# Performance work log

Hardware: AMD Instinct MI355X
Metric: run time of the kernel (lower is better)

Reference implementation:

```python
import jax, jax.numpy as jnp
import numpy as np

B, L, H, N = 16, 4096, 256, 64
N2 = N // 2


def setup_inputs() -> dict:
    key = jax.random.key(0)
    ks = jax.random.split(key, 12)
    x = jax.random.normal(ks[0], (B, L, H), dtype=jnp.float32)
    # S4D kernel params (S4D-Lin init)
    log_dt = jax.random.uniform(ks[1], (H,), dtype=jnp.float32) * (
        np.log(0.1) - np.log(0.001)) + np.log(0.001)
    log_A_real = jnp.full((H, N2), jnp.log(0.5), dtype=jnp.float32)
    A_imag = jnp.broadcast_to(np.pi * jnp.arange(N2, dtype=jnp.float32), (H, N2)).copy()
    C_re = jax.random.normal(ks[2], (H, N2), dtype=jnp.float32) * (0.5 ** 0.5)
    C_im = jax.random.normal(ks[3], (H, N2), dtype=jnp.float32) * (0.5 ** 0.5)
    D = jax.random.normal(ks[4], (H,), dtype=jnp.float32)
    # LayerNorm + 2-layer MLP params
    ln_g = jnp.ones((H,), dtype=jnp.float32)
    ln_b = jnp.zeros((H,), dtype=jnp.float32)
    s = 1.0 / np.sqrt(H)
    W1 = jax.random.uniform(ks[5], (H, H), dtype=jnp.float32, minval=-s, maxval=s)
    b1 = jax.random.uniform(ks[6], (H,), dtype=jnp.float32, minval=-s, maxval=s)
    W2 = jax.random.uniform(ks[7], (H, H), dtype=jnp.float32, minval=-s, maxval=s)
    b2 = jax.random.uniform(ks[8], (H,), dtype=jnp.float32, minval=-s, maxval=s)
    return dict(x=x, log_dt=log_dt, log_A_real=log_A_real, A_imag=A_imag,
                C_re=C_re, C_im=C_im, D=D, ln_g=ln_g, ln_b=ln_b,
                W1=W1, b1=b1, W2=W2, b2=b2)


def _s4d_kernel(log_dt, log_A_real, A_imag, C_re, C_im, length):
    # Returns real convolution kernel of shape (H, length)
    dt = jnp.exp(log_dt)                                  # (H,)
    A = -jnp.exp(log_A_real) + 1j * A_imag                # (H, N2) complex
    C = (C_re + 1j * C_im).astype(jnp.complex64)
    dtA = A * dt[:, None]                                 # (H, N2)
    # Discretization (ZOH-like): C * (exp(dtA) - 1) / A
    Cd = C * (jnp.exp(dtA) - 1.0) / A                     # (H, N2)
    t = jnp.arange(length, dtype=jnp.float32)
    vand = jnp.exp(dtA[:, :, None] * t)                   # (H, N2, L) complex Vandermonde
    K = 2.0 * jnp.einsum('hn,hnl->hl', Cd, vand).real     # (H, L)
    return K


def _forward(x, log_dt, log_A_real, A_imag, C_re, C_im, D,
             ln_g, ln_b, W1, b1, W2, b2):
    Bsz, Lseq, Hdim = x.shape
    K = _s4d_kernel(log_dt, log_A_real, A_imag, C_re, C_im, Lseq)  # (H, L)
    u = jnp.transpose(x, (0, 2, 1))                       # (B, H, L)
    n_fft = 2 * Lseq
    k_f = jnp.fft.rfft(K, n=n_fft)                        # (H, n_fft//2+1)
    u_f = jnp.fft.rfft(u, n=n_fft)                        # (B, H, n_fft//2+1)
    y = jnp.fft.irfft(u_f * k_f, n=n_fft)[..., :Lseq]     # causal conv (B, H, L)
    y = y + u * D[None, :, None]                          # skip connection
    y = jnp.transpose(y, (0, 2, 1))                       # (B, L, H)
    # LayerNorm over H
    mu = jnp.mean(y, axis=-1, keepdims=True)
    var = jnp.mean(jnp.square(y - mu), axis=-1, keepdims=True)
    y = (y - mu) * jax.lax.rsqrt(var + 1e-5) * ln_g + ln_b
    # Linear -> ReLU -> Linear -> ReLU (dropout is identity in eval)
    y = jax.nn.relu(jnp.einsum('blh,oh->blo', y, W1) + b1)
    y = jax.nn.relu(jnp.einsum('blh,oh->blo', y, W2) + b2)
    return x + y


def reference(x, log_dt, log_A_real, A_imag, C_re, C_im, D,
              ln_g, ln_b, W1, b1, W2, b2):
    return _forward(x, log_dt, log_A_real, A_imag, C_re, C_im, D,
                    ln_g, ln_b, W1, b1, W2, b2)
```

## Files before the change

kernel.cpp:

```cpp
#include <hip/hip_runtime.h>

#define H_DIM 256
#define N2D   32
#define L_SEQ 4096
#define B_SZ  16
#define L_C   128
#define N_C   32
#define KPAD  136

typedef short short8 __attribute__((ext_vector_type(8)));
typedef short short4v __attribute__((ext_vector_type(4)));
typedef float f32x4  __attribute__((ext_vector_type(4)));
typedef unsigned short ushort;

__device__ __forceinline__ ushort f2bf(float f) {
  unsigned int u = __float_as_uint(f);
  u = (u + 0x7fffu + ((u >> 16) & 1u)) >> 16;
  return (ushort)u;
}
__device__ __forceinline__ float bf2f(ushort s) {
  return __uint_as_float(((unsigned int)s) << 16);
}

__global__ __launch_bounds__(256) void k_front(
    const float* __restrict__ x, const float* __restrict__ log_dt,
    const float* __restrict__ log_A_real, const float* __restrict__ A_imag,
    const float* __restrict__ C_re, const float* __restrict__ C_im,
    const float* __restrict__ W1, const float* __restrict__ W2,
    const float* __restrict__ gam, const float* __restrict__ bet,
    const float* __restrict__ b1, float* __restrict__ parK,
    ushort* __restrict__ Mb, ushort* __restrict__ Lb,
    ushort* __restrict__ w1f, ushort* __restrict__ w2f,
    float* __restrict__ cs1, float* __restrict__ b1p,
    ushort* __restrict__ U) {
  int bid = blockIdx.x;
  int t = threadIdx.x;
  if (bid < 256) {
    int h = bid;
    __shared__ float sdre[32], sdim[32], scdr[32], scdi[32], slr[32], sli[32];
    if (t < 32) {
      int i = h * 32 + t;
      float dt = expf(log_dt[h]);
      float ar = -expf(log_A_real[i]);
      float ai = A_imag[i];
      float dre = ar * dt, dim = ai * dt;
      float er = expf(dre), sn, cs;
      sincosf(dim, &sn, &cs);
      float lr = er * cs, li = er * sn;
      float nr = lr - 1.f, ni = li;
      float inv = 1.f / (ar * ar + ai * ai);
      float tr = (nr * ar + ni * ai) * inv, ti = (ni * ar - nr * ai) * inv;
      float cdr = C_re[i] * tr - C_im[i] * ti;
      float cdi = C_re[i] * ti + C_im[i] * tr;
      sdre[t] = dre; sdim[t] = dim; scdr[t] = cdr; scdi[t] = cdi;
      slr[t] = lr; sli[t] = li;
      float e1 = expf(128.f * dre), ph = 128.f * dim;
      sincosf(ph, &sn, &cs);
      parK[i] = e1 * cs;
      parK[8192 + i] = e1 * sn;
    }
    __syncthreads();
    if (t < 128) {
      float ksum = 0.f;
      float tf = (float)t;
      for (int n = 0; n < 32; ++n) {
        float e = expf(tf * sdre[n]);
        float sn, cs;
        sincosf(tf * sdim[n], &sn, &cs);
        float pr = e * cs, pi = e * sn;
        ksum = fmaf(scdr[n], pr, fmaf(-scdi[n], pi, ksum));
        Lb[((size_t)h * 64 + 2 * n) * 128 + (127 - t)] = f2bf(pr);
        Lb[((size_t)h * 64 + 2 * n + 1) * 128 + (127 - t)] = f2bf(pi);
        float plr = pr * slr[n] - pi * sli[n];
        float pli = pr * sli[n] + pi * slr[n];
        Mb[((size_t)h * 128 + t) * 64 + 2 * n] =
            f2bf(2.f * (scdr[n] * plr - scdi[n] * pli));
        Mb[((size_t)h * 128 + t) * 64 + 2 * n + 1] =
            f2bf(-2.f * (scdr[n] * pli + scdi[n] * plr));
      }
      parK[16384 + h * 128 + t] = 2.f * ksum;
    }
  } else if (bid < 576) {
    int wb = bid - 256;
    if (wb < 64) {
      int i = wb * 256 + t;
      int mat = i >> 13;
      int fi = i & 8191;
      int l = fi & 63;
      int gk = fi >> 6;
      int g = gk & 15, kk = gk >> 4;
      int srow = mat ? ((g >> 2) * 64 + (l & 15) * 4 + (g & 3))
                     : (g * 16 + (l & 15));
      int scol = kk * 32 + ((l >> 4) << 3);
      const float* W = mat ? W2 : W1;
      ushort* out = mat ? w2f : w1f;
      short8 v;
#pragma unroll
      for (int e = 0; e < 8; ++e) {
        float w = W[(size_t)srow * 256 + scol + e];
        if (!mat) w *= gam[scol + e];
        v[e] = (short)f2bf(w);
      }
      *(short8*)&out[(size_t)fi * 8] = v;
    } else {
      int o = wb - 64;
      __shared__ float ra[256], rb[256];
      float w = W1[(size_t)o * 256 + t];
      ra[t] = bf2f(f2bf(w * gam[t]));
      rb[t] = w * bet[t];
      __syncthreads();
      for (int s = 128; s > 0; s >>= 1) {
        if (t < s) { ra[t] += ra[t + s]; rb[t] += rb[t + s]; }
        __syncthreads();
      }
      if (t == 0) { cs1[o] = ra[0]; b1p[o] = b1[o] + rb[0]; }
    }
  } else {
    int blk = bid - 576;
    int b = blk >> 7;
    int l0 = (blk & 127) << 5;
    __shared__ float tile[32][257];
#pragma unroll 8
    for (int r = 0; r < 32; ++r)
      tile[r][t] = x[((size_t)b * L_SEQ + l0 + r) * H_DIM + t];
    __syncthreads();
    int hq = t >> 2, ls = (t & 3) * 8;
#pragma unroll
    for (int pass = 0; pass < 4; ++pass) {
      int h = pass * 64 + hq;
      short8 v;
#pragma unroll
      for (int j = 0; j < 8; ++j) v[j] = (short)f2bf(tile[ls + j][h]);
      *(short8*)&U[(size_t)h * 65536 + (size_t)b * L_SEQ + l0 + ls] = v;
    }
  }
}

__global__ __launch_bounds__(256, 2) void k_sy(
    const ushort* __restrict__ U, const ushort* __restrict__ Lb,
    const float* __restrict__ parK, const ushort* __restrict__ Mb,
    const float* __restrict__ Dp, ushort* __restrict__ Uo) {
  int wgid = (blockIdx.x & 7) * 128 + (blockIdx.x >> 3);
  int h = wgid >> 2, ct = wgid & 3;
  int t = threadIdx.x;
  int lane = t & 63, wid = t >> 6;
  int wm = wid & 1, wn = wid >> 1;
  int lr_ = lane & 15, lk = (lane >> 4) << 3;
  __shared__ ushort Bt[128][KPAD];
  __shared__ __attribute__((aligned(16))) ushort ovl[18432];
  __shared__ float Krow[128];
  ushort (*sts)[72] = (ushort(*)[72])ovl;
  ushort (*M_lds)[72] = (ushort(*)[72])(ovl + 128 * 72);
  ushort (*T_lds)[136] = (ushort(*)[136])ovl;
  if (t < 128) {
    float kv = parK[16384 + h * 128 + t];
    if (t == 0) kv += Dp[h];
    Krow[t] = kv;
  }
#pragma unroll
  for (int q = 0; q < 8; ++q) {
    int idx = q * 256 + t;
    int cc = idx >> 4, seg = idx & 15;
    int col = ct * 128 + cc;
    int b = col >> 5, c = col & 31;
    *(short8*)&Bt[cc][seg * 8] = *(const short8*)&U[
        (size_t)h * 65536 + (size_t)b * L_SEQ + c * L_C + seg * 8];
  }
#pragma unroll
  for (int q = 0; q < 4; ++q) {
    int idx = q * 256 + t;
    int r = idx >> 3, seg = idx & 7;
    *(short8*)&M_lds[r][seg * 8] =
        *(const short8*)&Mb[((size_t)h * 128 + r) * 64 + seg * 8];
  }
  __syncthreads();
  {
    f32x4 acc2[4][2];
#pragma unroll
    for (int m = 0; m < 4; ++m)
#pragma unroll
      for (int n = 0; n < 2; ++n) acc2[m][n] = (f32x4){0.f, 0.f, 0.f, 0.f};
#pragma unroll
    for (int ks = 0; ks < 4; ++ks) {
      int k0 = ks * 32;
      short8 a[4], bfr[2];
#pragma unroll
      for (int m = 0; m < 4; ++m)
        a[m] = *(const short8*)&Bt[wm * 64 + m * 16 + lr_][k0 + lk];
#pragma unroll
      for (int n = 0; n < 2; ++n)
        bfr[n] = *(const short8*)&Lb[
            ((size_t)h * 64 + wn * 32 + n * 16 + lr_) * 128 + k0 + lk];
#pragma unroll
      for (int m = 0; m < 4; ++m)
#pragma unroll
        for (int n = 0; n < 2; ++n)
          acc2[m][n] = __builtin_amdgcn_mfma_f32_16x16x32_bf16(
              a[m], bfr[n], acc2[m][n], 0, 0, 0);
    }
#pragma unroll
    for (int m = 0; m < 4; ++m)
#pragma unroll
      for (int n = 0; n < 2; ++n)
#pragma unroll
        for (int jj = 0; jj < 4; ++jj) {
          int rowl = wm * 64 + m * 16 + (lane >> 4) * 4 + jj;
          int col2n = wn * 32 + n * 16 + (lane & 15);
          sts[rowl][col2n] = f2bf(acc2[m][n][jj]);
        }
  }
  __syncthreads();
  if (t < 128) {
    int n = t & 31, bl = t >> 5;
    float Lr = parK[h * 32 + n], Li = parK[8192 + h * 32 + n];
    float cr = 0.f, ci = 0.f;
#pragma unroll
    for (int c = 0; c < N_C; ++c) {
      int rowl = bl * 32 + c;
      uint* p = (uint*)&sts[rowl][2 * n];
      uint v = *p;
      float fr = bf2f((ushort)(v & 0xffff));
      float fi = bf2f((ushort)(v >> 16));
      *p = (uint)f2bf(cr) | ((uint)f2bf(ci) << 16);
      float nr_ = fmaf(Lr, cr, fmaf(-Li, ci, fr));
      float ni_ = fmaf(Lr, ci, fmaf(Li, cr, fi));
      cr = nr_; ci = ni_;
    }
  }
  __syncthreads();
  f32x4 acc[4][4];
#pragma unroll
  for (int m = 0; m < 4; ++m)
#pragma unroll
    for (int n = 0; n < 4; ++n) acc[m][n] = (f32x4){0.f, 0.f, 0.f, 0.f};
#pragma unroll
  for (int ks = 0; ks < 2; ++ks) {
    int k0 = ks * 32;
    short8 a[4], bfr[4];
#pragma unroll
    for (int m = 0; m < 4; ++m)
      a[m] = *(const short8*)&sts[wm * 64 + m * 16 + lr_][k0 + lk];
#pragma unroll
    for (int n = 0; n < 4; ++n)
      bfr[n] = *(const short8*)&M_lds[wn * 64 + n * 16 + lr_][k0 + lk];
#pragma unroll
    for (int m = 0; m < 4; ++m)
#pragma unroll
      for (int n = 0; n < 4; ++n)
        acc[m][n] = __builtin_amdgcn_mfma_f32_16x16x32_bf16(a[m], bfr[n],
                                                            acc[m][n], 0, 0, 0);
  }
  __syncthreads();
#pragma unroll
  for (int q = 0; q < 8; ++q) {
    int idx = q * 256 + t;
    int r = idx >> 4, seg = idx & 15;
    short8 v;
#pragma unroll
    for (int e = 0; e < 8; ++e) {
      int d = r - (seg * 8 + e);
      float f = (d >= 0) ? Krow[d] : 0.f;
      v[e] = (short)f2bf(f);
    }
    *(short8*)&T_lds[r][seg * 8] = v;
  }
  __syncthreads();
#pragma unroll
  for (int ks = 0; ks < 4; ++ks) {
    int k0 = ks * 32;
    short8 a[4], bfr[4];
#pragma unroll
    for (int m = 0; m < 4; ++m)
      a[m] = *(const short8*)&Bt[wm * 64 + m * 16 + lr_][k0 + lk];
#pragma unroll
    for (int n = 0; n < 4; ++n)
      bfr[n] = *(const short8*)&T_lds[wn * 64 + n * 16 + lr_][k0 + lk];
#pragma unroll
    for (int m = 0; m < 4; ++m)
#pragma unroll
      for (int n = 0; n < 4; ++n)
        acc[m][n] = __builtin_amdgcn_mfma_f32_16x16x32_bf16(a[m], bfr[n],
                                                            acc[m][n], 0, 0, 0);
  }
  __syncthreads();
#pragma unroll
  for (int m = 0; m < 4; ++m) {
    int rowl = wm * 64 + m * 16 + (lane >> 4) * 4;
#pragma unroll
    for (int jj = 0; jj < 4; ++jj) {
      int row = rowl + jj;
#pragma unroll
      for (int n = 0; n < 4; ++n) {
        int lp = wn * 64 + n * 16 + (lane & 15);
        Bt[row][lp] = f2bf(acc[m][n][jj]);
      }
    }
  }
  __syncthreads();
#pragma unroll
  for (int q = 0; q < 8; ++q) {
    int idx = q * 256 + t;
    int r = idx >> 4, seg = idx & 15;
    int col = ct * 128 + r;
    int b = col >> 5, c = col & 31;
    *(short8*)&Uo[(size_t)h * 65536 + (size_t)b * L_SEQ + c * L_C + seg * 8] =
        *(const short8*)&Bt[r][seg * 8];
  }
}

__global__ __launch_bounds__(512, 4) void k_mlp(
    const ushort* __restrict__ U, const ushort* __restrict__ w1f,
    const ushort* __restrict__ w2f, const float* __restrict__ cs1,
    const float* __restrict__ b1p, const float* __restrict__ b2,
    const float* __restrict__ xres, float* __restrict__ outp) {
  int m0 = blockIdx.x << 7;
  int t = threadIdx.x;
  int lane = t & 63, wid = t >> 6;
  int wm = wid & 1, wn = wid >> 1;
  int lr_ = lane & 15, lk = (lane >> 4) << 3;
  __shared__ ushort smem[33792];
  __shared__ float redA[128][4], redB[128][4];
  __shared__ float mu_s[128], rs_s[128];
  {
    int hseg = t >> 4, l16 = t & 15;
    int sw = (l16 & 7) << 3;
#pragma unroll
    for (int p = 0; p < 8; ++p) {
      int h = p * 32 + hseg;
      short8 v = *(const short8*)&U[(size_t)h * 65536 + m0 + l16 * 8];
      int hx = h ^ sw;
#pragma unroll
      for (int e = 0; e < 8; ++e)
        smem[(l16 * 8 + e) * 264 + hx] = (ushort)v[e];
    }
  }
  __syncthreads();
  {
    int rl = t >> 2, q = (t & 3) << 6;
    float s = 0.f, s2 = 0.f;
#pragma unroll
    for (int e = 0; e < 64; e += 8) {
      short8 v = *(const short8*)&smem[rl * 264 + q + e];
#pragma unroll
      for (int j = 0; j < 8; ++j) {
        float f = bf2f((ushort)v[j]);
        s += f;
        s2 = fmaf(f, f, s2);
      }
    }
    redA[rl][t & 3] = s;
    redB[rl][t & 3] = s2;
  }
  __syncthreads();
  if (t < 128) {
    float ss = redA[t][0] + redA[t][1] + redA[t][2] + redA[t][3];
    float ss2 = redB[t][0] + redB[t][1] + redB[t][2] + redB[t][3];
    float mu = ss * (1.f / 256.f);
    float var = fmaf(ss2, 1.f / 256.f, -mu * mu);
    mu_s[t] = mu;
    rs_s[t] = rsqrtf(var + 1e-5f);
  }
  __syncthreads();
  f32x4 acc[4][4];
#pragma unroll
  for (int m = 0; m < 4; ++m)
#pragma unroll
    for (int n = 0; n < 4; ++n) acc[m][n] = (f32x4){0.f, 0.f, 0.f, 0.f};
#pragma unroll
  for (int kabs = 0; kabs < 8; ++kabs) {
    short8 af[4], bfr[4];
#pragma unroll
    for (int n = 0; n < 4; ++n)
      bfr[n] = *(const short8*)&w1f[(((size_t)kabs * 16 + wn * 4 + n) * 64 +
                                     lane) * 8];
#pragma unroll
    for (int m = 0; m < 4; ++m) {
      int row = wm * 64 + m * 16 + lr_;
      int sw = ((row >> 3) & 7) << 3;
      af[m] = *(const short8*)&smem[row * 264 + ((kabs * 32 + lk) ^ sw)];
    }
#pragma unroll
    for (int m = 0; m < 4; ++m)
#pragma unroll
      for (int n = 0; n < 4; ++n)
        acc[m][n] = __builtin_amdgcn_mfma_f32_16x16x32_bf16(af[m], bfr[n],
                                                            acc[m][n], 0, 0, 0);
  }
  __syncthreads();
  int prow = (lane >> 4) << 2;
  int pcol = lane & 15;
#pragma unroll
  for (int n = 0; n < 4; ++n) {
    int gcol = wn * 64 + n * 16 + pcol;
    float c1v = cs1[gcol], b1v = b1p[gcol];
#pragma unroll
    for (int m = 0; m < 4; ++m) {
      int rbase = wm * 64 + m * 16 + prow;
#pragma unroll
      for (int j = 0; j < 4; ++j) {
        int row = rbase + j;
        float v = fmaxf(
            fmaf(rs_s[row], acc[m][n][j] - mu_s[row] * c1v, b1v), 0.f);
        int byte = ((row << 9) + (gcol << 1)) ^ ((row & 7) << 4);
        smem[byte >> 1] = f2bf(v);
        acc[m][n][j] = 0.f;
      }
    }
  }
  __syncthreads();
#pragma unroll
  for (int kabs = 0; kabs < 8; ++kabs) {
    short8 af[4], bfr[4];
#pragma unroll
    for (int n = 0; n < 4; ++n)
      bfr[n] = *(const short8*)&w2f[(((size_t)kabs * 16 + wn * 4 + n) * 64 +
                                     lane) * 8];
#pragma unroll
    for (int m = 0; m < 4; ++m) {
      int row = wm * 64 + m * 16 + lr_;
      int byte = ((row << 9) + ((kabs * 32 + lk) << 1)) ^ ((row & 7) << 4);
      af[m] = *(const short8*)&smem[byte >> 1];
    }
#pragma unroll
    for (int m = 0; m < 4; ++m)
#pragma unroll
      for (int n = 0; n < 4; ++n)
        acc[m][n] = __builtin_amdgcn_mfma_f32_16x16x32_bf16(af[m], bfr[n],
                                                            acc[m][n], 0, 0, 0);
  }
  f32x4 bv2q = *(const f32x4*)&b2[wn * 64 + pcol * 4];
#pragma unroll
  for (int m = 0; m < 4; ++m) {
#pragma unroll
    for (int j = 0; j < 4; ++j) {
      int grow = m0 + wm * 64 + m * 16 + prow + j;
      size_t base = (size_t)grow * 256 + wn * 64 + pcol * 4;
      f32x4 xr = *(const f32x4*)&xres[base];
      f32x4 o;
#pragma unroll
      for (int n = 0; n < 4; ++n)
        o[n] = xr[n] + fmaxf(acc[m][n][j] + bv2q[n], 0.f);
      *(f32x4*)&outp[base] = o;
    }
  }
}

extern "C" void kernel_launch(void* const* d_in, const int* in_sizes, int n_in,
                              void* d_out, int out_size, void* d_ws, size_t ws_size,
                              hipStream_t stream) {
  const float* x          = (const float*)d_in[0];
  const float* log_dt     = (const float*)d_in[1];
  const float* log_A_real = (const float*)d_in[2];
  const float* A_imag     = (const float*)d_in[3];
  const float* C_re       = (const float*)d_in[4];
  const float* C_im       = (const float*)d_in[5];
  const float* Dp         = (const float*)d_in[6];
  const float* ln_g       = (const float*)d_in[7];
  const float* ln_b       = (const float*)d_in[8];
  const float* W1         = (const float*)d_in[9];
  const float* b1         = (const float*)d_in[10];
  const float* W2         = (const float*)d_in[11];
  const float* b2         = (const float*)d_in[12];

  char* ws = (char*)d_ws;
  float* parK = (float*)ws;
  float* cs1  = (float*)(ws + 0x30000);
  float* b1p  = (float*)(ws + 0x30400);
  ushort* w1f = (ushort*)(ws + 0x40000);
  ushort* w2f = (ushort*)(ws + 0x60000);
  ushort* Mb  = (ushort*)(ws + 0x80000);
  ushort* Lb  = (ushort*)(ws + 0x480000);
  ushort* U   = (ushort*)(ws + 0x2080000);

  k_front<<<2624, 256, 0, stream>>>(x, log_dt, log_A_real, A_imag, C_re, C_im,
                                    W1, W2, ln_g, ln_b, b1, parK, Mb, Lb,
                                    w1f, w2f, cs1, b1p, U);
  k_sy<<<1024, 256, 0, stream>>>(U, Lb, parK, Mb, Dp, U);
  k_mlp<<<512, 512, 0, stream>>>(U, w1f, w2f, cs1, b1p, b2, x,
                                 (float*)d_out);
}
```

Before: 93.41 us.

## Split MLP block into two 64-row chunks with prefetch and lighter barriers

The k_mlp kernel now handles its 128 rows as two 64-row chunks. The U loads for the second chunk are prefetched into registers while the first chunk is processed, and the residual x loads are issued before the first GEMM. LayerNorm statistics are reduced with wave shuffles instead of shared-memory partial arrays. __syncthreads is replaced by an lgkmcnt wait plus s_barrier, and the LDS layout gets a new XOR swizzle with less padding. The goal is to overlap global loads with compute and cut LDS and register use, at the cost of more barrier phases and smaller per-chunk MFMA tiles.

```diff
diff --git a/kernel.cpp b/kernel.cpp
--- a/kernel.cpp
+++ b/kernel.cpp
@@ -20,6 +20,10 @@
 }
 __device__ __forceinline__ float bf2f(ushort s) {
   return __uint_as_float(((unsigned int)s) << 16);
+}
+__device__ __forceinline__ void barlg() {
+  asm volatile("s_waitcnt lgkmcnt(0)" ::: "memory");
+  __builtin_amdgcn_s_barrier();
 }
 
 __global__ __launch_bounds__(256) void k_front(
@@ -318,129 +322,153 @@
   int lane = t & 63, wid = t >> 6;
   int wm = wid & 1, wn = wid >> 1;
   int lr_ = lane & 15, lk = (lane >> 4) << 3;
-  __shared__ ushort smem[33792];
-  __shared__ float redA[128][4], redB[128][4];
-  __shared__ float mu_s[128], rs_s[128];
-  {
-    int hseg = t >> 4, l16 = t & 15;
-    int sw = (l16 & 7) << 3;
-#pragma unroll
-    for (int p = 0; p < 8; ++p) {
-      int h = p * 32 + hseg;
-      short8 v = *(const short8*)&U[(size_t)h * 65536 + m0 + l16 * 8];
-      int hx = h ^ sw;
-#pragma unroll
-      for (int e = 0; e < 8; ++e)
-        smem[(l16 * 8 + e) * 264 + hx] = (ushort)v[e];
-    }
-  }
-  __syncthreads();
-  {
-    int rl = t >> 2, q = (t & 3) << 6;
-    float s = 0.f, s2 = 0.f;
-#pragma unroll
-    for (int e = 0; e < 64; e += 8) {
-      short8 v = *(const short8*)&smem[rl * 264 + q + e];
-#pragma unroll
-      for (int j = 0; j < 8; ++j) {
-        float f = bf2f((ushort)v[j]);
-        s += f;
-        s2 = fmaf(f, f, s2);
-      }
-    }
-    redA[rl][t & 3] = s;
-    redB[rl][t & 3] = s2;
-  }
-  __syncthreads();
-  if (t < 128) {
-    float ss = redA[t][0] + redA[t][1] + redA[t][2] + redA[t][3];
-    float ss2 = redB[t][0] + redB[t][1] + redB[t][2] + redB[t][3];
-    float mu = ss * (1.f / 256.f);
-    float var = fmaf(ss2, 1.f / 256.f, -mu * mu);
-    mu_s[t] = mu;
-    rs_s[t] = rsqrtf(var + 1e-5f);
-  }
-  __syncthreads();
-  f32x4 acc[4][4];
-#pragma unroll
-  for (int m = 0; m < 4; ++m)
-#pragma unroll
-    for (int n = 0; n < 4; ++n) acc[m][n] = (f32x4){0.f, 0.f, 0.f, 0.f};
-#pragma unroll
-  for (int kabs = 0; kabs < 8; ++kabs) {
-    short8 af[4], bfr[4];
-#pragma unroll
-    for (int n = 0; n < 4; ++n)
-      bfr[n] = *(const short8*)&w1f[(((size_t)kabs * 16 + wn * 4 + n) * 64 +
-                                     lane) * 8];
-#pragma unroll
-    for (int m = 0; m < 4; ++m) {
-      int row = wm * 64 + m * 16 + lr_;
-      int sw = ((row >> 3) & 7) << 3;
-      af[m] = *(const short8*)&smem[row * 264 + ((kabs * 32 + lk) ^ sw)];
-    }
-#pragma unroll
-    for (int m = 0; m < 4; ++m)
-#pragma unroll
-      for (int n = 0; n < 4; ++n)
-        acc[m][n] = __builtin_amdgcn_mfma_f32_16x16x32_bf16(af[m], bfr[n],
-                                                            acc[m][n], 0, 0, 0);
-  }
-  __syncthreads();
-  int prow = (lane >> 4) << 2;
-  int pcol = lane & 15;
+  __shared__ __attribute__((aligned(16))) ushort sm[32768];
+  __shared__ float mu_s[64], rs_s[64];
+  int prow = (lane >> 4) << 2, pcol = lane & 15;
+  float c1v[4], b1v[4];
 #pragma unroll
   for (int n = 0; n < 4; ++n) {
     int gcol = wn * 64 + n * 16 + pcol;
-    float c1v = cs1[gcol], b1v = b1p[gcol];
-#pragma unroll
-    for (int m = 0; m < 4; ++m) {
-      int rbase = wm * 64 + m * 16 + prow;
+    c1v[n] = cs1[gcol];
+    b1v[n] = b1p[gcol];
+  }
+  f32x4 b2q = *(const f32x4*)&b2[wn * 64 + pcol * 4];
+  int hseg = t >> 3, l8 = t & 7;
+  short8 uv[4];
+#pragma unroll
+  for (int p = 0; p < 4; ++p)
+    uv[p] = *(const short8*)&U[(size_t)(p * 64 + hseg) * 65536 + m0 + l8 * 8];
+#pragma unroll
+  for (int c = 0; c < 2; ++c) {
+    int mc = m0 + c * 64;
+#pragma unroll
+    for (int p = 0; p < 4; ++p) {
+      int h = p * 64 + hseg;
+#pragma unroll
+      for (int e = 0; e < 8; ++e) {
+        int m = l8 * 8 + e;
+        int byte = m * 512 + ((h * 2) ^ ((e ^ l8) << 4));
+        sm[byte >> 1] = (ushort)uv[p][e];
+      }
+    }
+    if (c == 0) {
+#pragma unroll
+      for (int p = 0; p < 4; ++p)
+        uv[p] = *(const short8*)&U[(size_t)(p * 64 + hseg) * 65536 + m0 + 64 +
+                                   l8 * 8];
+    }
+    barlg();
+    {
+      int row = t >> 3, c8 = t & 7;
+      int fr = ((row & 7) ^ ((row >> 3) & 7)) << 4;
+      float s = 0.f, s2 = 0.f;
+#pragma unroll
+      for (int e = 0; e < 4; ++e) {
+        int byte = row * 512 + (((c8 + e * 8) * 16) ^ fr);
+        short8 v = *(const short8*)&sm[byte >> 1];
+#pragma unroll
+        for (int j = 0; j < 8; ++j) {
+          float f = bf2f((ushort)v[j]);
+          s += f;
+          s2 = fmaf(f, f, s2);
+        }
+      }
+#pragma unroll
+      for (int d = 1; d < 8; d <<= 1) {
+        s += __shfl_xor(s, d);
+        s2 += __shfl_xor(s2, d);
+      }
+      if (c8 == 0) {
+        float mu = s * (1.f / 256.f);
+        float var = fmaf(s2, 1.f / 256.f, -mu * mu);
+        mu_s[row] = mu;
+        rs_s[row] = rsqrtf(var + 1e-5f);
+      }
+    }
+    barlg();
+    f32x4 xr[2][4];
+#pragma unroll
+    for (int m = 0; m < 2; ++m)
+#pragma unroll
+      for (int j = 0; j < 4; ++j)
+        xr[m][j] = *(const f32x4*)&xres[
+            (size_t)(mc + wm * 32 + m * 16 + prow + j) * 256 + wn * 64 +
+            pcol * 4];
+    f32x4 acc[2][4];
+#pragma unroll
+    for (int m = 0; m < 2; ++m)
+#pragma unroll
+      for (int n = 0; n < 4; ++n) acc[m][n] = (f32x4){0.f, 0.f, 0.f, 0.f};
+#pragma unroll
+    for (int kabs = 0; kabs < 8; ++kabs) {
+      short8 af[2], bfr[4];
+#pragma unroll
+      for (int n = 0; n < 4; ++n)
+        bfr[n] = *(const short8*)&w1f[(((size_t)kabs * 16 + wn * 4 + n) * 64 +
+                                       lane) * 8];
+#pragma unroll
+      for (int m = 0; m < 2; ++m) {
+        int row = wm * 32 + m * 16 + lr_;
+        int fr = ((row & 7) ^ ((row >> 3) & 7)) << 4;
+        af[m] = *(const short8*)&sm[(row * 512 + ((kabs * 64 + lk * 2) ^ fr)) >>
+                                    1];
+      }
+#pragma unroll
+      for (int m = 0; m < 2; ++m)
+#pragma unroll
+        for (int n = 0; n < 4; ++n)
+          acc[m][n] = __builtin_amdgcn_mfma_f32_16x16x32_bf16(af[m], bfr[n],
+                                                              acc[m][n], 0, 0, 0);
+    }
+#pragma unroll
+    for (int n = 0; n < 4; ++n) {
+      int gcol = wn * 64 + n * 16 + pcol;
+#pragma unroll
+      for (int m = 0; m < 2; ++m) {
+#pragma unroll
+        for (int j = 0; j < 4; ++j) {
+          int row = wm * 32 + m * 16 + prow + j;
+          float v = fmaxf(
+              fmaf(rs_s[row], acc[m][n][j] - mu_s[row] * c1v[n], b1v[n]), 0.f);
+          int byte = ((row << 9) + (gcol << 1)) ^ ((row & 7) << 4);
+          sm[16384 + (byte >> 1)] = f2bf(v);
+          acc[m][n][j] = 0.f;
+        }
+      }
+    }
+    barlg();
+#pragma unroll
+    for (int kabs = 0; kabs < 8; ++kabs) {
+      short8 af[2], bfr[4];
+#pragma unroll
+      for (int n = 0; n < 4; ++n)
+        bfr[n] = *(const short8*)&w2f[(((size_t)kabs * 16 + wn * 4 + n) * 64 +
+                                       lane) * 8];
+#pragma unroll
+      for (int m = 0; m < 2; ++m) {
+        int row = wm * 32 + m * 16 + lr_;
+        int byte = ((row << 9) + ((kabs * 32 + lk) << 1)) ^ ((row & 7) << 4);
+        af[m] = *(const short8*)&sm[16384 + (byte >> 1)];
+      }
+#pragma unroll
+      for (int m = 0; m < 2; ++m)
+#pragma unroll
+        for (int n = 0; n < 4; ++n)
+          acc[m][n] = __builtin_amdgcn_mfma_f32_16x16x32_bf16(af[m], bfr[n],
+                                                              acc[m][n], 0, 0, 0);
+    }
+#pragma unroll
+    for (int m = 0; m < 2; ++m) {
 #pragma unroll
       for (int j = 0; j < 4; ++j) {
-        int row = rbase + j;
-        float v = fmaxf(
-            fmaf(rs_s[row], acc[m][n][j] - mu_s[row] * c1v, b1v), 0.f);
-        int byte = ((row << 9) + (gcol << 1)) ^ ((row & 7) << 4);
-        smem[byte >> 1] = f2bf(v);
-        acc[m][n][j] = 0.f;
-      }
-    }
-  }
-  __syncthreads();
-#pragma unroll
-  for (int kabs = 0; kabs < 8; ++kabs) {
-    short8 af[4], bfr[4];
-#pragma unroll
-    for (int n = 0; n < 4; ++n)
-      bfr[n] = *(const short8*)&w2f[(((size_t)kabs * 16 + wn * 4 + n) * 64 +
-                                     lane) * 8];
-#pragma unroll
-    for (int m = 0; m < 4; ++m) {
-      int row = wm * 64 + m * 16 + lr_;
-      int byte = ((row << 9) + ((kabs * 32 + lk) << 1)) ^ ((row & 7) << 4);
-      af[m] = *(const short8*)&smem[byte >> 1];
-    }
-#pragma unroll
-    for (int m = 0; m < 4; ++m)
-#pragma unroll
-      for (int n = 0; n < 4; ++n)
-        acc[m][n] = __builtin_amdgcn_mfma_f32_16x16x32_bf16(af[m], bfr[n],
-                                                            acc[m][n], 0, 0, 0);
-  }
-  f32x4 bv2q = *(const f32x4*)&b2[wn * 64 + pcol * 4];
-#pragma unroll
-  for (int m = 0; m < 4; ++m) {
-#pragma unroll
-    for (int j = 0; j < 4; ++j) {
-      int grow = m0 + wm * 64 + m * 16 + prow + j;
-      size_t base = (size_t)grow * 256 + wn * 64 + pcol * 4;
-      f32x4 xr = *(const f32x4*)&xres[base];
-      f32x4 o;
-#pragma unroll
-      for (int n = 0; n < 4; ++n)
-        o[n] = xr[n] + fmaxf(acc[m][n][j] + bv2q[n], 0.f);
-      *(f32x4*)&outp[base] = o;
+        size_t base = (size_t)(mc + wm * 32 + m * 16 + prow + j) * 256 +
+                      wn * 64 + pcol * 4;
+        f32x4 o;
+#pragma unroll
+        for (int n = 0; n < 4; ++n)
+          o[n] = xr[m][j][n] + fmaxf(acc[m][n][j] + b2q[n], 0.f);
+        *(f32x4*)&outp[base] = o;
+      }
     }
   }
 }
```

New measurement: 195.9 us. 110% more time.
